# Performance work log

Measured on AMD Instinct MI355X. Metric: run time of the kernel, lower is better.

Reference implementation:

```python
import jax, jax.numpy as jnp
import numpy as np

SQRT_N = 64  # sqrt_n; padded sequence length n = SQRT_N**2 = 4096


def _perm(x, r):
    # rearrange '... (m n) -> ... (n m)' with m = n = r
    return x.reshape(*x.shape[:-1], r, r).swapaxes(-1, -2).reshape(x.shape)


def _blockdiag_matmul(x, w):
    # torch.einsum('bnm,...bm->...bn', w, x.view(..., b, m)).reshape(x.shape)
    b, _, m = w.shape
    xv = x.reshape(*x.shape[:-1], b, m)
    return jnp.einsum('bnm,...bm->...bn', w, xv).reshape(x.shape)


def _monarch(x, L, R, r):
    x = _perm(x, r)
    x = _blockdiag_matmul(x, L)
    x = _perm(x, r)
    x = _blockdiag_matmul(x, R)
    return _perm(x, r)


def setup_inputs() -> dict:
    key = jax.random.key(0)
    ks = jax.random.split(key, 9)
    B, S, H, D = 8, 4096, 8, 64
    r = SQRT_N
    bound_b = 1.0 / r
    # kaiming_uniform_(a=sqrt(5)) on a (r, r, r) tensor: fan_in = r*r,
    # gain = sqrt(2/(1+5)) = sqrt(1/3), bound = gain*sqrt(3/fan_in) = 1/r
    bound_w = 1.0 / r
    return {
        'queries': jax.random.normal(ks[0], (B, S, H, D), jnp.float32),
        'keys': jax.random.normal(ks[1], (B, S, H, D), jnp.float32),
        'values': jax.random.normal(ks[2], (B, S, H, D), jnp.float32),
        'M1L': jax.random.uniform(ks[3], (r, r, r), jnp.float32, -bound_w, bound_w),
        'M1R': jax.random.uniform(ks[4], (r, r, r), jnp.float32, -bound_w, bound_w),
        'M2L': jax.random.uniform(ks[5], (r, r, r), jnp.float32, -bound_w, bound_w),
        'M2R': jax.random.uniform(ks[6], (r, r, r), jnp.float32, -bound_w, bound_w),
        'b1': jax.random.uniform(ks[7], (r * r,), jnp.float32, -bound_b, bound_b),
        'b2': jax.random.uniform(ks[8], (r * r,), jnp.float32, -bound_b, bound_b),
    }


def reference(queries, keys, values, M1L, M1R, M2L, M2R, b1, b2):
    r = SQRT_N
    B, S, H, D = queries.shape
    n2 = r * r
    pad = n2 - S
    # (B,S,H,D) -> (B,H,D,S)
    q = jnp.transpose(queries, (0, 2, 3, 1))
    k = jnp.transpose(keys, (0, 2, 3, 1))
    v = jnp.transpose(values, (0, 2, 3, 1))
    cfg = [(0, 0)] * 3 + [(0, pad)]
    q = jnp.pad(q, cfg)
    k = jnp.pad(k, cfg)
    # A = M1(q) * k + b1 ; dropout is identity (eval / p=0)
    A = _monarch(q, M1L, M1R, r) * k + b1
    A = _monarch(A, M2L, M2R, r) + b2
    Y = A[..., :S] * v  # (B,H,D,S)
    return Y
```

## Files before the change

kernel.cpp:

```cpp
#include <hip/hip_runtime.h>
#include <cstdint>
#include <cstddef>

typedef unsigned short u16;
typedef __attribute__((ext_vector_type(8))) short bf16x8;
typedef __attribute__((ext_vector_type(4))) float f32x4;

#define S_LEN 4096

__device__ __forceinline__ float bf2f(u16 u) {
  return __uint_as_float(((unsigned)u) << 16);
}
__device__ __forceinline__ u16 f2bf(float f) {
  unsigned x = __float_as_uint(f);
  return (u16)((x + 0x7fffu + ((x >> 16) & 1u)) >> 16);
}

__device__ __forceinline__ int ltelem(int c, int r) {
  int swz = ((r >> 3) ^ (c & 7) ^ ((c >> 3) & 7)) & 7;
  return (c << 6) | (swz << 3) | (r & 7);
}

__device__ __forceinline__ bf16x8 load_bfrag(const ushort* LT, int fc, int ks, int lane) {
  int c = (fc << 4) + (lane & 15);
  int kg = (ks << 2) + (lane >> 4);
  int base = (c << 6) | (((kg ^ (c & 7) ^ ((c >> 3) & 7)) & 7) << 3);
  return *(const bf16x8*)&LT[base];
}

__device__ __forceinline__ bf16x8 apk_frag(const u16* __restrict__ APK, int mat, int gr,
                                           int ks, int lane) {
  return *(const bf16x8*)&APK[(((((mat << 8) + gr) << 1) + ks) << 9) + lane * 8];
}

__device__ __forceinline__ void mm16x64(const u16* __restrict__ APK, int mat, int gr,
                                        const ushort* LT, int lane, f32x4 acc[4]) {
#pragma unroll
  for (int ks = 0; ks < 2; ++ks) {
    bf16x8 af = apk_frag(APK, mat, gr, ks, lane);
#pragma unroll
    for (int fc = 0; fc < 4; ++fc) {
      bf16x8 bf = load_bfrag(LT, fc, ks, lane);
      acc[fc] = __builtin_amdgcn_mfma_f32_16x16x32_bf16(af, bf, acc[fc], 0, 0, 0);
    }
  }
}

__global__ __launch_bounds__(256) void k_prep(const float* __restrict__ W0,
                                              const float* __restrict__ W1,
                                              const float* __restrict__ W2,
                                              const float* __restrict__ W3,
                                              u16* __restrict__ APK) {
  const int gr = blockIdx.x, mat = blockIdx.y;
  const float* W = (mat == 0) ? W0 : (mat == 1) ? W1 : (mat == 2) ? W2 : W3;
  const int t = threadIdx.x;
  const int lane = t & 63, ks = (t >> 6) & 1, half = t >> 7;
  const int row = gr * 16 + (lane & 15);
  const int k0 = ks * 32 + ((lane >> 4) << 3) + half * 4;
  float4 v = *(const float4*)&W[row * 64 + k0];
  ushort4 o;
  o.x = f2bf(v.x); o.y = f2bf(v.y); o.z = f2bf(v.z); o.w = f2bf(v.w);
  *(ushort4*)&APK[((((((mat << 8) + gr) << 1) + ks) << 6) + lane) * 8 + half * 4] = o;
}

__global__ __launch_bounds__(256) void k_m1(const float* __restrict__ q,
                                            const u16* __restrict__ APK,
                                            u16* __restrict__ T1) {
  const int B = blockIdx.x, bh = blockIdx.y;
  const int b = bh >> 3, h = bh & 7;
  __shared__ ushort LT[4096];
  const int tid = threadIdx.x, w = tid >> 6, lane = tid & 63;
  {
    const int m = tid >> 2, ch = tid & 3;
    const float* qrow = q + ((((size_t)b * S_LEN + (size_t)m * 64 + B) * 8 + h) << 6);
#pragma unroll
    for (int i = 0; i < 4; ++i) {
      float4 v = *(const float4*)(qrow + ch * 16 + i * 4);
      int c0 = ch * 16 + i * 4;
      LT[ltelem(c0 + 0, m)] = f2bf(v.x);
      LT[ltelem(c0 + 1, m)] = f2bf(v.y);
      LT[ltelem(c0 + 2, m)] = f2bf(v.z);
      LT[ltelem(c0 + 3, m)] = f2bf(v.w);
    }
  }
  __syncthreads();
  f32x4 acc[4] = {};
  mm16x64(APK, 0, B * 4 + w, LT, lane, acc);
#pragma unroll
  for (int fc = 0; fc < 4; ++fc) {
    int d = (fc << 4) + (lane & 15);
#pragma unroll
    for (int r = 0; r < 4; ++r) {
      int n = (w << 4) + ((lane >> 4) << 2) + r;
      T1[(((size_t)bh * 64 + n) * 64 + B) * 64 + d] = f2bf(acc[fc][r]);
    }
  }
}

__global__ __launch_bounds__(256) void k_m2b(const u16* __restrict__ T1,
                                             const u16* __restrict__ APK,
                                             const float* __restrict__ keys,
                                             const float* __restrict__ b1,
                                             u16* __restrict__ T2) {
  const int n = blockIdx.x, bh = blockIdx.y;
  const int b = bh >> 3, h = bh & 7;
  __shared__ ushort LT[4096];
  __shared__ ushort LT2[4096];
  const int tid = threadIdx.x, w = tid >> 6, lane = tid & 63;

  float kreg[4][4], b1v[4];
#pragma unroll
  for (int r = 0; r < 4; ++r) {
    int p = (w << 4) + ((lane >> 4) << 2) + r;
    b1v[r] = b1[p * 64 + n];
    const float* krow = &keys[(((size_t)b * S_LEN + p * 64 + n) * 8 + h) << 6];
#pragma unroll
    for (int fc = 0; fc < 4; ++fc)
      kreg[fc][r] = krow[(fc << 4) + (lane & 15)];
  }
  {
    const int rowi = tid >> 2, ch = tid & 3;
    const u16* src = T1 + (((size_t)bh * 64 + n) * 64 + rowi) * 64 + ch * 16;
    u16 buf[16];
    *(uint4*)&buf[0] = *(const uint4*)(src);
    *(uint4*)&buf[8] = *(const uint4*)(src + 8);
#pragma unroll
    for (int e = 0; e < 16; ++e) LT[ltelem(ch * 16 + e, rowi)] = buf[e];
  }
  __syncthreads();
  f32x4 acc[4] = {};
  mm16x64(APK, 1, n * 4 + w, LT, lane, acc);
#pragma unroll
  for (int fc = 0; fc < 4; ++fc) {
    int d = (fc << 4) + (lane & 15);
#pragma unroll
    for (int r = 0; r < 4; ++r) {
      int p = (w << 4) + ((lane >> 4) << 2) + r;
      LT2[ltelem(d, p)] = f2bf(acc[fc][r] * kreg[fc][r] + b1v[r]);
    }
  }
  __syncthreads();
  f32x4 acc2[4] = {};
  mm16x64(APK, 2, n * 4 + w, LT2, lane, acc2);
#pragma unroll
  for (int fc = 0; fc < 4; ++fc) {
    int d = (fc << 4) + (lane & 15);
#pragma unroll
    for (int r = 0; r < 4; ++r) {
      int n2 = (w << 4) + ((lane >> 4) << 2) + r;
      T2[(((size_t)bh * 64 + n2) * 64 + n) * 64 + d] = f2bf(acc2[fc][r]);
    }
  }
}

__global__ __launch_bounds__(256) void k_m3b(const u16* __restrict__ T2,
                                             const u16* __restrict__ APK,
                                             const float* __restrict__ vals,
                                             const float* __restrict__ b2,
                                             u16* __restrict__ Yp) {
  const int np = blockIdx.x, bh = blockIdx.y;
  const int b = bh >> 3, h = bh & 7;
  __shared__ ushort LT[4096];
  const int tid = threadIdx.x, w = tid >> 6, lane = tid & 63;

  float vreg[4][4], b2v[4];
#pragma unroll
  for (int r = 0; r < 4; ++r) {
    int p = (w << 4) + ((lane >> 4) << 2) + r;
    b2v[r] = b2[p * 64 + np];
    const float* vrow = &vals[(((size_t)b * S_LEN + p * 64 + np) * 8 + h) << 6];
#pragma unroll
    for (int fc = 0; fc < 4; ++fc)
      vreg[fc][r] = vrow[(fc << 4) + (lane & 15)];
  }
  {
    const int rowi = tid >> 2, ch = tid & 3;
    const u16* src = T2 + (((size_t)bh * 64 + np) * 64 + rowi) * 64 + ch * 16;
    u16 buf[16];
    *(uint4*)&buf[0] = *(const uint4*)(src);
    *(uint4*)&buf[8] = *(const uint4*)(src + 8);
#pragma unroll
    for (int e = 0; e < 16; ++e) LT[ltelem(ch * 16 + e, rowi)] = buf[e];
  }
  __syncthreads();
  f32x4 acc[4] = {};
  mm16x64(APK, 3, np * 4 + w, LT, lane, acc);
#pragma unroll
  for (int fc = 0; fc < 4; ++fc) {
    int d = (fc << 4) + (lane & 15);
#pragma unroll
    for (int r = 0; r < 4; ++r) {
      int p = (w << 4) + ((lane >> 4) << 2) + r;
      Yp[(((size_t)bh * 64 + np) * 64 + p) * 64 + d] = f2bf((acc[fc][r] + b2v[r]) * vreg[fc][r]);
    }
  }
}

__global__ __launch_bounds__(256) void k_tr(const u16* __restrict__ Yp,
                                            float* __restrict__ out) {
  const int p = blockIdx.x, bh = blockIdx.y;
  __shared__ ushort YT[4096];
  const int tid = threadIdx.x;
#pragma unroll
  for (int i = 0; i < 2; ++i) {
    int idx = i * 256 + tid;
    int np = idx >> 3, q8 = idx & 7;
    uint4 vv = *(const uint4*)&Yp[(((size_t)bh * 64 + np) * 64 + p) * 64 + q8 * 8];
    *(uint4*)&YT[ltelem(np, q8 * 8)] = vv;
  }
  __syncthreads();
#pragma unroll
  for (int i = 0; i < 4; ++i) {
    int idx = i * 256 + tid;
    int d = idx >> 4, np0 = (idx & 15) * 4;
    float4 o;
    o.x = bf2f(YT[ltelem(np0 + 0, d)]);
    o.y = bf2f(YT[ltelem(np0 + 1, d)]);
    o.z = bf2f(YT[ltelem(np0 + 2, d)]);
    o.w = bf2f(YT[ltelem(np0 + 3, d)]);
    *(float4*)&out[((size_t)bh * 64 + d) * S_LEN + p * 64 + np0] = o;
  }
}

extern "C" void kernel_launch(void* const* d_in, const int* in_sizes, int n_in,
                              void* d_out, int out_size, void* d_ws, size_t ws_size,
                              hipStream_t stream) {
  const float* q   = (const float*)d_in[0];
  const float* k   = (const float*)d_in[1];
  const float* v   = (const float*)d_in[2];
  const float* M1L = (const float*)d_in[3];
  const float* M1R = (const float*)d_in[4];
  const float* M2L = (const float*)d_in[5];
  const float* M2R = (const float*)d_in[6];
  const float* b1  = (const float*)d_in[7];
  const float* b2  = (const float*)d_in[8];

  u16* T1 = (u16*)d_ws;
  u16* T2 = T1 + (size_t)64 * 64 * 64 * 64;
  u16* Yp = T1;
  u16* APK = (u16*)d_out;

  dim3 blk(256);
  dim3 grd(64, 64);
  k_prep<<<dim3(256, 4), blk, 0, stream>>>(M1L, M1R, M2L, M2R, APK);
  k_m1 <<<grd, blk, 0, stream>>>(q, APK, T1);
  k_m2b<<<grd, blk, 0, stream>>>(T1, APK, k, b1, T2);
  k_m3b<<<grd, blk, 0, stream>>>(T2, APK, v, b2, Yp);
  k_tr <<<grd, blk, 0, stream>>>(Yp, (float*)d_out);
}
```

Baseline: 109.4 us.

## Fuse all monarch stages into one kernel keeping intermediates in LDS

Replaces the four stage kernels (M1, M2+bias, M3, transpose) with a single mega-kernel. Each 512-thread block owns 16 head-dim columns of one (b,h) and keeps the whole 64x64x16 bf16 intermediate in shared memory, so the bf16 round trips through global workspace T1/T2/Yp go away. The first input permutation is folded into the prepacked M1L weights, and packed bf16 conversion is used. In exchange the grid shrinks to 256 blocks, each using about 144KB of LDS at one block per CU, so occupancy and latency hiding drop and the k/v gathers become strided scalar loads.

```diff
diff --git a/kernel.cpp b/kernel.cpp
--- a/kernel.cpp
+++ b/kernel.cpp
@@ -6,8 +6,6 @@
 typedef __attribute__((ext_vector_type(8))) short bf16x8;
 typedef __attribute__((ext_vector_type(4))) float f32x4;
 
-#define S_LEN 4096
-
 __device__ __forceinline__ float bf2f(u16 u) {
   return __uint_as_float(((unsigned)u) << 16);
 }
@@ -15,17 +13,17 @@
   unsigned x = __float_as_uint(f);
   return (u16)((x + 0x7fffu + ((x >> 16) & 1u)) >> 16);
 }
-
-__device__ __forceinline__ int ltelem(int c, int r) {
-  int swz = ((r >> 3) ^ (c & 7) ^ ((c >> 3) & 7)) & 7;
-  return (c << 6) | (swz << 3) | (r & 7);
-}
-
-__device__ __forceinline__ bf16x8 load_bfrag(const ushort* LT, int fc, int ks, int lane) {
-  int c = (fc << 4) + (lane & 15);
-  int kg = (ks << 2) + (lane >> 4);
-  int base = (c << 6) | (((kg ^ (c & 7) ^ ((c >> 3) & 7)) & 7) << 3);
-  return *(const bf16x8*)&LT[base];
+__device__ __forceinline__ unsigned pk2(float a, float b) {
+  unsigned r;
+  asm("v_cvt_pk_bf16_f32 %0, %1, %2" : "=v"(r) : "v"(a), "v"(b));
+  return r;
+}
+
+__device__ __forceinline__ int taddr(int g, int dl, int x) {
+  return (((g << 4) + dl) << 6) + (x ^ (((g ^ dl) & 7) << 3));
+}
+__device__ __forceinline__ int saddr(int w, int dl, int p) {
+  return 65536 + (((w << 4) + dl) << 6) + (p ^ ((dl & 7) << 3));
 }
 
 __device__ __forceinline__ bf16x8 apk_frag(const u16* __restrict__ APK, int mat, int gr,
@@ -33,16 +31,21 @@
   return *(const bf16x8*)&APK[(((((mat << 8) + gr) << 1) + ks) << 9) + lane * 8];
 }
 
-__device__ __forceinline__ void mm16x64(const u16* __restrict__ APK, int mat, int gr,
-                                        const ushort* LT, int lane, f32x4 acc[4]) {
-#pragma unroll
-  for (int ks = 0; ks < 2; ++ks) {
-    bf16x8 af = apk_frag(APK, mat, gr, ks, lane);
-#pragma unroll
-    for (int fc = 0; fc < 4; ++fc) {
-      bf16x8 bf = load_bfrag(LT, fc, ks, lane);
-      acc[fc] = __builtin_amdgcn_mfma_f32_16x16x32_bf16(af, bf, acc[fc], 0, 0, 0);
-    }
+__device__ __forceinline__ bf16x8 xfrag(const ushort* Xs, int g, int ks, int lane) {
+  return *(const bf16x8*)&Xs[taddr(g, lane & 15, ((ks << 2) + (lane >> 4)) << 3)];
+}
+__device__ __forceinline__ bf16x8 sfrag(const ushort* Xs, int w, int ks, int lane) {
+  return *(const bf16x8*)&Xs[saddr(w, lane & 15, ((ks << 2) + (lane >> 4)) << 3)];
+}
+
+__device__ __forceinline__ void wmm(const u16* __restrict__ APK, int mat, int unit,
+                                    bf16x8 f0, bf16x8 f1, int lane, f32x4 acc[4]) {
+#pragma unroll
+  for (int grp = 0; grp < 4; ++grp) {
+    acc[grp] = __builtin_amdgcn_mfma_f32_16x16x32_bf16(
+        apk_frag(APK, mat, unit * 4 + grp, 0, lane), f0, acc[grp], 0, 0, 0);
+    acc[grp] = __builtin_amdgcn_mfma_f32_16x16x32_bf16(
+        apk_frag(APK, mat, unit * 4 + grp, 1, lane), f1, acc[grp], 0, 0, 0);
   }
 }
 
@@ -57,168 +60,169 @@
   const int lane = t & 63, ks = (t >> 6) & 1, half = t >> 7;
   const int row = gr * 16 + (lane & 15);
   const int k0 = ks * 32 + ((lane >> 4) << 3) + half * 4;
-  float4 v = *(const float4*)&W[row * 64 + k0];
   ushort4 o;
-  o.x = f2bf(v.x); o.y = f2bf(v.y); o.z = f2bf(v.z); o.w = f2bf(v.w);
+  if (mat == 0) {
+    o.x = f2bf(W[row * 64 + ((((k0 + 0) & 7) << 3) | ((k0 + 0) >> 3))]);
+    o.y = f2bf(W[row * 64 + ((((k0 + 1) & 7) << 3) | ((k0 + 1) >> 3))]);
+    o.z = f2bf(W[row * 64 + ((((k0 + 2) & 7) << 3) | ((k0 + 2) >> 3))]);
+    o.w = f2bf(W[row * 64 + ((((k0 + 3) & 7) << 3) | ((k0 + 3) >> 3))]);
+  } else {
+    float4 v = *(const float4*)&W[row * 64 + k0];
+    o.x = f2bf(v.x); o.y = f2bf(v.y); o.z = f2bf(v.z); o.w = f2bf(v.w);
+  }
   *(ushort4*)&APK[((((((mat << 8) + gr) << 1) + ks) << 6) + lane) * 8 + half * 4] = o;
 }
 
-__global__ __launch_bounds__(256) void k_m1(const float* __restrict__ q,
-                                            const u16* __restrict__ APK,
-                                            u16* __restrict__ T1) {
-  const int B = blockIdx.x, bh = blockIdx.y;
+__global__ __launch_bounds__(512, 1) void k_mega(const float* __restrict__ q,
+                                                 const float* __restrict__ keys,
+                                                 const float* __restrict__ vals,
+                                                 const u16* __restrict__ APK,
+                                                 const float* __restrict__ b1,
+                                                 const float* __restrict__ b2,
+                                                 float* __restrict__ out) {
+  __shared__ ushort Xs[73728];
+  const int dq = blockIdx.x, bh = blockIdx.y;
   const int b = bh >> 3, h = bh & 7;
-  __shared__ ushort LT[4096];
-  const int tid = threadIdx.x, w = tid >> 6, lane = tid & 63;
+  const int tid = threadIdx.x, w = tid >> 6, l = tid & 63;
+  const size_t inbase = (size_t)b * 4096 * 512 + h * 64 + dq * 16;
+
   {
-    const int m = tid >> 2, ch = tid & 3;
-    const float* qrow = q + ((((size_t)b * S_LEN + (size_t)m * 64 + B) * 8 + h) << 6);
-#pragma unroll
-    for (int i = 0; i < 4; ++i) {
-      float4 v = *(const float4*)(qrow + ch * 16 + i * 4);
-      int c0 = ch * 16 + i * 4;
-      LT[ltelem(c0 + 0, m)] = f2bf(v.x);
-      LT[ltelem(c0 + 1, m)] = f2bf(v.y);
-      LT[ltelem(c0 + 2, m)] = f2bf(v.z);
-      LT[ltelem(c0 + 3, m)] = f2bf(v.w);
+    const int B = l;
+#pragma unroll
+    for (int hh = 0; hh < 2; ++hh) {
+      float st[4][16];
+#pragma unroll
+      for (int jj = 0; jj < 4; ++jj) {
+        const int m = w + 8 * (hh * 4 + jj);
+        const float* qr = q + inbase + (size_t)(m * 64 + B) * 512;
+        float4 v0 = *(const float4*)(qr);
+        float4 v1 = *(const float4*)(qr + 4);
+        float4 v2 = *(const float4*)(qr + 8);
+        float4 v3 = *(const float4*)(qr + 12);
+        st[jj][0] = v0.x;  st[jj][1] = v0.y;  st[jj][2] = v0.z;  st[jj][3] = v0.w;
+        st[jj][4] = v1.x;  st[jj][5] = v1.y;  st[jj][6] = v1.z;  st[jj][7] = v1.w;
+        st[jj][8] = v2.x;  st[jj][9] = v2.y;  st[jj][10] = v2.z; st[jj][11] = v2.w;
+        st[jj][12] = v3.x; st[jj][13] = v3.y; st[jj][14] = v3.z; st[jj][15] = v3.w;
+      }
+#pragma unroll
+      for (int dl = 0; dl < 16; ++dl) {
+        uint2 pw;
+        pw.x = pk2(st[0][dl], st[1][dl]);
+        pw.y = pk2(st[2][dl], st[3][dl]);
+        *(uint2*)&Xs[taddr(B, dl, w * 8 + hh * 4)] = pw;
+      }
     }
   }
   __syncthreads();
-  f32x4 acc[4] = {};
-  mm16x64(APK, 0, B * 4 + w, LT, lane, acc);
-#pragma unroll
-  for (int fc = 0; fc < 4; ++fc) {
-    int d = (fc << 4) + (lane & 15);
-#pragma unroll
-    for (int r = 0; r < 4; ++r) {
-      int n = (w << 4) + ((lane >> 4) << 2) + r;
-      T1[(((size_t)bh * 64 + n) * 64 + B) * 64 + d] = f2bf(acc[fc][r]);
+
+  bf16x8 fr[8][2];
+
+#pragma unroll
+  for (int u = 0; u < 8; ++u) {
+    fr[u][0] = xfrag(Xs, w * 8 + u, 0, l);
+    fr[u][1] = xfrag(Xs, w * 8 + u, 1, l);
+  }
+  __syncthreads();
+#pragma unroll
+  for (int u = 0; u < 8; ++u) {
+    const int B = w * 8 + u;
+    f32x4 acc[4] = {};
+    wmm(APK, 0, B, fr[u][0], fr[u][1], l, acc);
+#pragma unroll
+    for (int grp = 0; grp < 4; ++grp)
+#pragma unroll
+      for (int r = 0; r < 4; ++r) {
+        const int n = grp * 16 + ((l >> 4) << 2) + r;
+        Xs[taddr(n, l & 15, B)] = f2bf(acc[grp][r]);
+      }
+  }
+  __syncthreads();
+
+#pragma unroll
+  for (int u = 0; u < 8; ++u) {
+    fr[u][0] = xfrag(Xs, w * 8 + u, 0, l);
+    fr[u][1] = xfrag(Xs, w * 8 + u, 1, l);
+  }
+  __syncthreads();
+#pragma unroll
+  for (int u = 0; u < 8; ++u) {
+    const int n = w * 8 + u;
+    float kreg[16], b1r[16];
+#pragma unroll
+    for (int grp = 0; grp < 4; ++grp)
+#pragma unroll
+      for (int r = 0; r < 4; ++r) {
+        const int y = grp * 16 + ((l >> 4) << 2) + r;
+        kreg[grp * 4 + r] = keys[inbase + (size_t)(y * 64 + n) * 512 + (l & 15)];
+        b1r[grp * 4 + r] = b1[y * 64 + n];
+      }
+    f32x4 acc[4] = {};
+    wmm(APK, 1, n, fr[u][0], fr[u][1], l, acc);
+#pragma unroll
+    for (int grp = 0; grp < 4; ++grp)
+#pragma unroll
+      for (int r = 0; r < 4; ++r) {
+        const int y = grp * 16 + ((l >> 4) << 2) + r;
+        Xs[saddr(w, l & 15, y)] = f2bf(acc[grp][r] * kreg[grp * 4 + r] + b1r[grp * 4 + r]);
+      }
+    bf16x8 s0 = sfrag(Xs, w, 0, l);
+    bf16x8 s1 = sfrag(Xs, w, 1, l);
+    f32x4 acc2[4] = {};
+    wmm(APK, 2, n, s0, s1, l, acc2);
+#pragma unroll
+    for (int grp = 0; grp < 4; ++grp)
+#pragma unroll
+      for (int r = 0; r < 4; ++r) {
+        const int n2 = grp * 16 + ((l >> 4) << 2) + r;
+        Xs[taddr(n2, l & 15, n)] = f2bf(acc2[grp][r]);
+      }
+  }
+  __syncthreads();
+
+#pragma unroll
+  for (int u = 0; u < 8; ++u) {
+    fr[u][0] = xfrag(Xs, w * 8 + u, 0, l);
+    fr[u][1] = xfrag(Xs, w * 8 + u, 1, l);
+  }
+  __syncthreads();
+#pragma unroll
+  for (int u = 0; u < 8; ++u) {
+    const int n2 = w * 8 + u;
+    float vreg[16], b2r[16];
+#pragma unroll
+    for (int grp = 0; grp < 4; ++grp)
+#pragma unroll
+      for (int r = 0; r < 4; ++r) {
+        const int y = grp * 16 + ((l >> 4) << 2) + r;
+        vreg[grp * 4 + r] = vals[inbase + (size_t)(y * 64 + n2) * 512 + (l & 15)];
+        b2r[grp * 4 + r] = b2[y * 64 + n2];
+      }
+    f32x4 acc[4] = {};
+    wmm(APK, 3, n2, fr[u][0], fr[u][1], l, acc);
+#pragma unroll
+    for (int grp = 0; grp < 4; ++grp)
+#pragma unroll
+      for (int r = 0; r < 4; ++r) {
+        const int i2 = grp * 16 + ((l >> 4) << 2) + r;
+        Xs[taddr(i2, l & 15, n2)] = f2bf((acc[grp][r] + b2r[grp * 4 + r]) * vreg[grp * 4 + r]);
+      }
+  }
+  __syncthreads();
+
+  {
+    const int dl = tid >> 5, c = tid & 31;
+    float* orow = out + ((size_t)bh * 64 + dq * 16 + dl) * 4096;
+#pragma unroll
+    for (int o = 0; o < 32; ++o) {
+      const int s4 = o * 128 + c * 4;
+      uint2 rv = *(const uint2*)&Xs[taddr(s4 >> 6, dl, s4 & 63)];
+      float4 ov;
+      ov.x = bf2f((u16)(rv.x & 0xffffu));
+      ov.y = bf2f((u16)(rv.x >> 16));
+      ov.z = bf2f((u16)(rv.y & 0xffffu));
+      ov.w = bf2f((u16)(rv.y >> 16));
+      *(float4*)(orow + s4) = ov;
     }
-  }
-}
-
-__global__ __launch_bounds__(256) void k_m2b(const u16* __restrict__ T1,
-                                             const u16* __restrict__ APK,
-                                             const float* __restrict__ keys,
-                                             const float* __restrict__ b1,
-                                             u16* __restrict__ T2) {
-  const int n = blockIdx.x, bh = blockIdx.y;
-  const int b = bh >> 3, h = bh & 7;
-  __shared__ ushort LT[4096];
-  __shared__ ushort LT2[4096];
-  const int tid = threadIdx.x, w = tid >> 6, lane = tid & 63;
-
-  float kreg[4][4], b1v[4];
-#pragma unroll
-  for (int r = 0; r < 4; ++r) {
-    int p = (w << 4) + ((lane >> 4) << 2) + r;
-    b1v[r] = b1[p * 64 + n];
-    const float* krow = &keys[(((size_t)b * S_LEN + p * 64 + n) * 8 + h) << 6];
-#pragma unroll
-    for (int fc = 0; fc < 4; ++fc)
-      kreg[fc][r] = krow[(fc << 4) + (lane & 15)];
-  }
-  {
-    const int rowi = tid >> 2, ch = tid & 3;
-    const u16* src = T1 + (((size_t)bh * 64 + n) * 64 + rowi) * 64 + ch * 16;
-    u16 buf[16];
-    *(uint4*)&buf[0] = *(const uint4*)(src);
-    *(uint4*)&buf[8] = *(const uint4*)(src + 8);
-#pragma unroll
-    for (int e = 0; e < 16; ++e) LT[ltelem(ch * 16 + e, rowi)] = buf[e];
-  }
-  __syncthreads();
-  f32x4 acc[4] = {};
-  mm16x64(APK, 1, n * 4 + w, LT, lane, acc);
-#pragma unroll
-  for (int fc = 0; fc < 4; ++fc) {
-    int d = (fc << 4) + (lane & 15);
-#pragma unroll
-    for (int r = 0; r < 4; ++r) {
-      int p = (w << 4) + ((lane >> 4) << 2) + r;
-      LT2[ltelem(d, p)] = f2bf(acc[fc][r] * kreg[fc][r] + b1v[r]);
-    }
-  }
-  __syncthreads();
-  f32x4 acc2[4] = {};
-  mm16x64(APK, 2, n * 4 + w, LT2, lane, acc2);
-#pragma unroll
-  for (int fc = 0; fc < 4; ++fc) {
-    int d = (fc << 4) + (lane & 15);
-#pragma unroll
-    for (int r = 0; r < 4; ++r) {
-      int n2 = (w << 4) + ((lane >> 4) << 2) + r;
-      T2[(((size_t)bh * 64 + n2) * 64 + n) * 64 + d] = f2bf(acc2[fc][r]);
-    }
-  }
-}
-
-__global__ __launch_bounds__(256) void k_m3b(const u16* __restrict__ T2,
-                                             const u16* __restrict__ APK,
-                                             const float* __restrict__ vals,
-                                             const float* __restrict__ b2,
-                                             u16* __restrict__ Yp) {
-  const int np = blockIdx.x, bh = blockIdx.y;
-  const int b = bh >> 3, h = bh & 7;
-  __shared__ ushort LT[4096];
-  const int tid = threadIdx.x, w = tid >> 6, lane = tid & 63;
-
-  float vreg[4][4], b2v[4];
-#pragma unroll
-  for (int r = 0; r < 4; ++r) {
-    int p = (w << 4) + ((lane >> 4) << 2) + r;
-    b2v[r] = b2[p * 64 + np];
-    const float* vrow = &vals[(((size_t)b * S_LEN + p * 64 + np) * 8 + h) << 6];
-#pragma unroll
-    for (int fc = 0; fc < 4; ++fc)
-      vreg[fc][r] = vrow[(fc << 4) + (lane & 15)];
-  }
-  {
-    const int rowi = tid >> 2, ch = tid & 3;
-    const u16* src = T2 + (((size_t)bh * 64 + np) * 64 + rowi) * 64 + ch * 16;
-    u16 buf[16];
-    *(uint4*)&buf[0] = *(const uint4*)(src);
-    *(uint4*)&buf[8] = *(const uint4*)(src + 8);
-#pragma unroll
-    for (int e = 0; e < 16; ++e) LT[ltelem(ch * 16 + e, rowi)] = buf[e];
-  }
-  __syncthreads();
-  f32x4 acc[4] = {};
-  mm16x64(APK, 3, np * 4 + w, LT, lane, acc);
-#pragma unroll
-  for (int fc = 0; fc < 4; ++fc) {
-    int d = (fc << 4) + (lane & 15);
-#pragma unroll
-    for (int r = 0; r < 4; ++r) {
-      int p = (w << 4) + ((lane >> 4) << 2) + r;
-      Yp[(((size_t)bh * 64 + np) * 64 + p) * 64 + d] = f2bf((acc[fc][r] + b2v[r]) * vreg[fc][r]);
-    }
-  }
-}
-
-__global__ __launch_bounds__(256) void k_tr(const u16* __restrict__ Yp,
-                                            float* __restrict__ out) {
-  const int p = blockIdx.x, bh = blockIdx.y;
-  __shared__ ushort YT[4096];
-  const int tid = threadIdx.x;
-#pragma unroll
-  for (int i = 0; i < 2; ++i) {
-    int idx = i * 256 + tid;
-    int np = idx >> 3, q8 = idx & 7;
-    uint4 vv = *(const uint4*)&Yp[(((size_t)bh * 64 + np) * 64 + p) * 64 + q8 * 8];
-    *(uint4*)&YT[ltelem(np, q8 * 8)] = vv;
-  }
-  __syncthreads();
-#pragma unroll
-  for (int i = 0; i < 4; ++i) {
-    int idx = i * 256 + tid;
-    int d = idx >> 4, np0 = (idx & 15) * 4;
-    float4 o;
-    o.x = bf2f(YT[ltelem(np0 + 0, d)]);
-    o.y = bf2f(YT[ltelem(np0 + 1, d)]);
-    o.z = bf2f(YT[ltelem(np0 + 2, d)]);
-    o.w = bf2f(YT[ltelem(np0 + 3, d)]);
-    *(float4*)&out[((size_t)bh * 64 + d) * S_LEN + p * 64 + np0] = o;
   }
 }
 
@@ -235,16 +239,8 @@
   const float* b1  = (const float*)d_in[7];
   const float* b2  = (const float*)d_in[8];
 
-  u16* T1 = (u16*)d_ws;
-  u16* T2 = T1 + (size_t)64 * 64 * 64 * 64;
-  u16* Yp = T1;
-  u16* APK = (u16*)d_out;
-
-  dim3 blk(256);
-  dim3 grd(64, 64);
-  k_prep<<<dim3(256, 4), blk, 0, stream>>>(M1L, M1R, M2L, M2R, APK);
-  k_m1 <<<grd, blk, 0, stream>>>(q, APK, T1);
-  k_m2b<<<grd, blk, 0, stream>>>(T1, APK, k, b1, T2);
-  k_m3b<<<grd, blk, 0, stream>>>(T2, APK, v, b2, Yp);
-  k_tr <<<grd, blk, 0, stream>>>(Yp, (float*)d_out);
-}
+  u16* APK = (u16*)d_ws;
+
+  k_prep<<<dim3(256, 4), 256, 0, stream>>>(M1L, M1R, M2L, M2R, APK);
+  k_mega<<<dim3(4, 64), 512, 0, stream>>>(q, k, v, APK, b1, b2, (float*)d_out);
+}
```

Result: slower. 316.1 us (+189.0%).
